# Kernel optimization log

Hardware: AMD Instinct MI355X
Metric: run time of the kernel (lower is better)

## Reference

```python
import jax, jax.numpy as jnp
import numpy as np

N, D, NS, HID = 65536, 256, 1024, 256
EPS = 1e-8
SCALE = D ** -0.5


def layer_norm(x, w, b, eps=1e-5):
    mu = jnp.mean(x, axis=-1, keepdims=True)
    var = jnp.mean(jnp.square(x - mu), axis=-1, keepdims=True)
    return (x - mu) * jax.lax.rsqrt(var + eps) * w + b


def mask_attn(attn, k):
    # per-row top-k mask, vectorized (replaces the torch Python loop)
    idx = jax.lax.top_k(attn, k)[1]                      # [rows, k]
    rows = jnp.arange(attn.shape[0])[:, None]
    mask = jnp.zeros(attn.shape, jnp.bool_).at[rows, idx].set(True)
    return attn * mask


def setup_inputs() -> dict:
    key = jax.random.key(0)
    ks = jax.random.split(key, 20)
    def lin_w(k, din, dout):
        return jax.random.normal(k, (din, dout), jnp.float32) * (1.0 / np.sqrt(din))
    return {
        "inputs": jax.random.normal(ks[0], (N, D), jnp.float32),
        "noise": jax.random.normal(ks[1], (NS, D), jnp.float32),
        "edges_mu": jax.random.normal(ks[2], (1, D), jnp.float32),
        "edges_logsigma": jax.random.uniform(ks[3], (1, D), jnp.float32, -0.1, 0.1),
        "wq": lin_w(ks[4], D, D), "bq": jnp.zeros((D,), jnp.float32),
        "wk": lin_w(ks[5], D, D), "bk": jnp.zeros((D,), jnp.float32),
        "wv": lin_w(ks[6], D, D), "bv": jnp.zeros((D,), jnp.float32),
        "mlp_w1": lin_w(ks[7], 2 * D, HID), "mlp_b1": jnp.zeros((HID,), jnp.float32),
        "mlp_w2": lin_w(ks[8], HID, D), "mlp_b2": jnp.zeros((D,), jnp.float32),
        "ln_in_w": jnp.ones((D,), jnp.float32), "ln_in_b": jnp.zeros((D,), jnp.float32),
        "ln_e_w": jnp.ones((D,), jnp.float32), "ln_e_b": jnp.zeros((D,), jnp.float32),
        "k_n": 512,
        "k_e": 32,
    }


def reference(inputs, noise, edges_mu, edges_logsigma, wq, bq, wk, bk, wv, bv,
              mlp_w1, mlp_b1, mlp_w2, mlp_b2, ln_in_w, ln_in_b, ln_e_w, ln_e_b,
              k_n, k_e):
    # slot init: mu + sigma * eps
    edges = edges_mu + jnp.exp(edges_logsigma) * noise            # [NS, D]
    x = layer_norm(inputs, ln_in_w, ln_in_b)                      # [N, D]
    k = jax.nn.relu(x @ wk + bk)                                  # [N, D]
    v = jax.nn.relu(x @ wv + bv)                                  # [N, D]

    # iters = 1 (single unrolled iteration, as in the default config)
    e = layer_norm(edges, ln_e_w, ln_e_b)                         # [NS, D]
    q = jax.nn.relu(e @ wq + bq)                                  # [NS, D]
    dots = (q @ k.T) * SCALE                                      # [NS, N]
    attn = jax.nn.softmax(dots, axis=1) + EPS
    attn = attn / jnp.sum(attn, axis=1, keepdims=True)
    attn = mask_attn(attn, k_n)
    updates = attn @ v                                            # [NS, D]
    edges = jax.nn.relu(jnp.concatenate([e, updates], axis=1) @ mlp_w1 + mlp_b1) @ mlp_w2 + mlp_b2  # [NS, D]

    q2 = x @ wq + bq                                              # [N, D] (no relu, as in source)
    k2 = jax.nn.relu(edges @ wk + bk)                             # [NS, D]
    dots2 = (q2 @ k2.T) * SCALE                                   # [N, NS]
    H = mask_attn(jax.nn.softmax(dots2, axis=1), k_e)             # [N, NS]
    return edges, H, dots2
```

## Files before the change

kernel.cpp:

```cpp
#include <hip/hip_runtime.h>
#include <hip/hip_bf16.h>
#include <stdint.h>


#define DEV __device__ __forceinline__

typedef uint32_t u32;
typedef uint16_t u16;
typedef __bf16 v8bf __attribute__((ext_vector_type(8)));
typedef float v4f __attribute__((ext_vector_type(4)));

static constexpr long NN = 65536;
static constexpr long DD = 256;
static constexpr long NSL = 1024;

DEV u16 f2b(float f) {
  u32 u = __builtin_bit_cast(u32, f);
  u32 r = (u + 0x7FFFu + ((u >> 16) & 1u)) >> 16;
  return (u16)r;
}
DEV float b2f(u16 h) { u32 u = ((u32)h) << 16; return __builtin_bit_cast(float, u); }
DEV u32 b2k(u32 b) { return b ^ (0x8000u + 0x7FFFu * (b >> 15)); }
DEV float k2fv(u32 k) {
  u16 b = (k & 0x8000u) ? (u16)(k ^ 0x8000u) : (u16)(k ^ 0xFFFFu);
  return b2f(b);
}

DEV void gl_lds16(const u16* g, u16* l) {
  __builtin_amdgcn_global_load_lds(
      (const __attribute__((address_space(1))) u32*)g,
      (__attribute__((address_space(3))) u32*)l, 16, 0, 0);
}

template <int EPI>
__global__ __launch_bounds__(256, 2)
void gemm_bt(const u16* __restrict__ A, const u16* __restrict__ B,
             const float* __restrict__ bias, float scale,
             u16* __restrict__ ob0, u16* __restrict__ ob1, u16* __restrict__ ob2,
             float* __restrict__ of) {
  __shared__ __align__(16) u16 smem[128 * 128];
  u16* As = smem;
  u16* Bs = smem + 128 * 64;
  const int tid = threadIdx.x;
  const int lane = tid & 63;
  const int l15 = lane & 15;
  const int l4 = lane >> 4;
  const int wid = tid >> 6;
  const int wm = wid >> 1, wn = wid & 1;
  const long m0 = (long)blockIdx.y * 128;
  const long n0 = (long)blockIdx.x * 128;

  v4f acc[4][4] = {};

  for (int kb = 0; kb < 256; kb += 64) {
    __syncthreads();
#pragma unroll
    for (int i = 0; i < 4; i++) {
      int cid = tid + 256 * i;
      int row = cid >> 3, ch = cid & 7;
      int sch = ch ^ (row & 7);
      gl_lds16(A + (m0 + row) * 256 + kb + sch * 8, &As[cid * 8]);
      gl_lds16(B + (n0 + row) * 256 + kb + sch * 8, &Bs[cid * 8]);
    }
    __syncthreads();
#pragma unroll
    for (int ks = 0; ks < 2; ks++) {
      v8bf af[4], bfr[4];
#pragma unroll
      for (int m = 0; m < 4; m++) {
        int row = wm * 64 + m * 16 + l15;
        int sch = (ks * 4 + l4) ^ (row & 7);
        af[m] = *reinterpret_cast<const v8bf*>(&As[row * 64 + sch * 8]);
      }
#pragma unroll
      for (int n = 0; n < 4; n++) {
        int row = wn * 64 + n * 16 + l15;
        int sch = (ks * 4 + l4) ^ (row & 7);
        bfr[n] = *reinterpret_cast<const v8bf*>(&Bs[row * 64 + sch * 8]);
      }
#pragma unroll
      for (int m = 0; m < 4; m++)
#pragma unroll
        for (int n = 0; n < 4; n++)
          acc[m][n] = __builtin_amdgcn_mfma_f32_16x16x32_bf16(af[m], bfr[n], acc[m][n], 0, 0, 0);
    }
  }

  const int r4 = l4 * 4;
  if constexpr (EPI == 3) {
#pragma unroll
    for (int m = 0; m < 4; m++)
#pragma unroll
      for (int n = 0; n < 4; n++)
#pragma unroll
        for (int r = 0; r < 4; r++) {
          long grow = m0 + wm * 64 + m * 16 + r4 + r;
          long gcol = n0 + wn * 64 + n * 16 + l15;
          of[grow * 1024 + gcol] = acc[m][n][r] * scale;
        }
  } else {
    __syncthreads();
#pragma unroll
    for (int m = 0; m < 4; m++) {
#pragma unroll
      for (int n = 0; n < 4; n++) {
#pragma unroll
        for (int r = 0; r < 4; r++) {
          int srow = wm * 64 + m * 16 + r4 + r;
          int scol = wn * 64 + n * 16 + l15;
          float v = acc[m][n][r];
          if constexpr (EPI == 0 || EPI == 1) {
            v += bias[n0 + scol];
          } else {
            v *= scale;
          }
          smem[srow * 128 + scol] = f2b(v);
        }
      }
    }
    __syncthreads();
    if constexpr (EPI == 0) {
      const int which = (int)(n0 >> 8);
      const long jj0 = n0 & 255;
      u16* ob = (which == 0) ? ob0 : (which == 1) ? ob1 : ob2;
      const bool dorelu = (which < 2);
#pragma unroll
      for (int i = 0; i < 8; i++) {
        int idx = tid + 256 * i;
        int row = idx >> 4, seg = idx & 15;
        uint4 t = *reinterpret_cast<const uint4*>(&smem[row * 128 + seg * 8]);
        if (dorelu) {
          u32* w = reinterpret_cast<u32*>(&t);
#pragma unroll
          for (int q = 0; q < 4; q++) {
            u32 lo16 = w[q] & 0xffffu, hi16 = w[q] >> 16;
            if (lo16 & 0x8000u) lo16 = 0;
            if (hi16 & 0x8000u) hi16 = 0;
            w[q] = lo16 | (hi16 << 16);
          }
        }
        *reinterpret_cast<uint4*>(&ob[(m0 + row) * 256 + jj0 + seg * 8]) = t;
      }
    } else if constexpr (EPI == 1) {
#pragma unroll
      for (int i = 0; i < 8; i++) {
        int idx = tid + 256 * i;
        int row = idx >> 4, seg = idx & 15;
        uint4 t = *reinterpret_cast<const uint4*>(&smem[row * 128 + seg * 8]);
        u32* w = reinterpret_cast<u32*>(&t);
#pragma unroll
        for (int q = 0; q < 4; q++) {
          u32 lo16 = w[q] & 0xffffu, hi16 = w[q] >> 16;
          if (lo16 & 0x8000u) lo16 = 0;
          if (hi16 & 0x8000u) hi16 = 0;
          w[q] = lo16 | (hi16 << 16);
        }
        *reinterpret_cast<uint4*>(&ob0[(m0 + row) * 256 + n0 + seg * 8]) = t;
      }
    } else {
#pragma unroll
      for (int i = 0; i < 8; i++) {
        int idx = tid + 256 * i;
        int row = idx >> 4, seg = idx & 15;
        uint4 t = *reinterpret_cast<const uint4*>(&smem[row * 128 + seg * 8]);
        *reinterpret_cast<uint4*>(&ob0[(m0 + row) * 65536 + n0 + seg * 8]) = t;
      }
    }
  }
}

__global__ __launch_bounds__(256)
void prep_w_kernel(const float* __restrict__ wq, const float* __restrict__ wk,
                   const float* __restrict__ wv, const float* __restrict__ bq,
                   const float* __restrict__ bk, const float* __restrict__ bv,
                   u16* __restrict__ wcat, float* __restrict__ bcat) {
  int n = blockIdx.x;
  int t = threadIdx.x;
  const float* W = (n < 256) ? wk : (n < 512) ? wv : wq;
  int jj = n & 255;
  wcat[n * 256 + t] = f2b(W[t * 256 + jj]);
  if (t == 0) {
    const float* Bb = (n < 256) ? bk : (n < 512) ? bv : bq;
    bcat[n] = Bb[jj];
  }
}

__global__ __launch_bounds__(256)
void ln_x_kernel(const float* __restrict__ x, const float* __restrict__ lw,
                 const float* __restrict__ lb, u16* __restrict__ out) {
  const int lane = threadIdx.x & 63, wid = threadIdx.x >> 6;
  const long row = (long)blockIdx.x * 4 + wid;
  float4 v = reinterpret_cast<const float4*>(x + row * 256)[lane];
  float s = v.x + v.y + v.z + v.w;
  for (int sh = 1; sh < 64; sh <<= 1) s += __shfl_xor(s, sh);
  float mu = s * (1.f / 256.f);
  float dx = v.x - mu, dy = v.y - mu, dz = v.z - mu, dw = v.w - mu;
  float q = dx * dx + dy * dy + dz * dz + dw * dw;
  for (int sh = 1; sh < 64; sh <<= 1) q += __shfl_xor(q, sh);
  float rs = rsqrtf(q * (1.f / 256.f) + 1e-5f);
  float4 wv = reinterpret_cast<const float4*>(lw)[lane];
  float4 bv = reinterpret_cast<const float4*>(lb)[lane];
  ushort4 o4;
  o4.x = f2b(dx * rs * wv.x + bv.x);
  o4.y = f2b(dy * rs * wv.y + bv.y);
  o4.z = f2b(dz * rs * wv.z + bv.z);
  o4.w = f2b(dw * rs * wv.w + bv.w);
  reinterpret_cast<ushort4*>(out + row * 256)[lane] = o4;
}

__global__ __launch_bounds__(256)
void edges_e_kernel(const float* __restrict__ noise, const float* __restrict__ emu,
                    const float* __restrict__ els, const float* __restrict__ lw,
                    const float* __restrict__ lb, float* __restrict__ e_f,
                    u16* __restrict__ e_b) {
  const int lane = threadIdx.x & 63, wid = threadIdx.x >> 6;
  const long row = (long)blockIdx.x * 4 + wid;
  float4 nz = reinterpret_cast<const float4*>(noise + row * 256)[lane];
  float4 mu4 = reinterpret_cast<const float4*>(emu)[lane];
  float4 ls4 = reinterpret_cast<const float4*>(els)[lane];
  float4 ed;
  ed.x = mu4.x + expf(ls4.x) * nz.x;
  ed.y = mu4.y + expf(ls4.y) * nz.y;
  ed.z = mu4.z + expf(ls4.z) * nz.z;
  ed.w = mu4.w + expf(ls4.w) * nz.w;
  float s = ed.x + ed.y + ed.z + ed.w;
  for (int sh = 1; sh < 64; sh <<= 1) s += __shfl_xor(s, sh);
  float mu = s * (1.f / 256.f);
  float dx = ed.x - mu, dy = ed.y - mu, dz = ed.z - mu, dw = ed.w - mu;
  float qv = dx * dx + dy * dy + dz * dz + dw * dw;
  for (int sh = 1; sh < 64; sh <<= 1) qv += __shfl_xor(qv, sh);
  float rs = rsqrtf(qv * (1.f / 256.f) + 1e-5f);
  float4 wv = reinterpret_cast<const float4*>(lw)[lane];
  float4 bv = reinterpret_cast<const float4*>(lb)[lane];
  float4 ef;
  ef.x = dx * rs * wv.x + bv.x;
  ef.y = dy * rs * wv.y + bv.y;
  ef.z = dz * rs * wv.z + bv.z;
  ef.w = dw * rs * wv.w + bv.w;
  reinterpret_cast<float4*>(e_f + row * 256)[lane] = ef;
  ushort4 o4;
  o4.x = f2b(ef.x); o4.y = f2b(ef.y); o4.z = f2b(ef.z); o4.w = f2b(ef.w);
  reinterpret_cast<ushort4*>(e_b + row * 256)[lane] = o4;
}

struct D2Shm {
  u32 hist[256 * 16];
  u32 c_hi[256];
  u32 sel_idx[1152];
  float sel_w[1152];
  float fred[4];
  u32 sb_star, sThi, sThr;
  float sSE, sFrac;
  u32 scnt;
};

__global__ __launch_bounds__(256, 5)
void d2d3_kernel(const u16* __restrict__ dots, const u16* __restrict__ vmat,
                 const int* __restrict__ knp, float* __restrict__ upd) {
  __shared__ D2Shm S;
  const int tid = threadIdx.x, lane = tid & 63, wid = tid >> 6;
  const int hc = (lane >> 2);
  const long r = blockIdx.x;
  const int kn = *knp;

  for (int i = tid; i < 4096; i += 256) S.hist[i] = 0;
  if (tid == 0) S.scnt = 0;
  __syncthreads();

  const float C = 8.f;
  const uint4* src = reinterpret_cast<const uint4*>(dots + r * 65536);

  float se = 0.f;
  for (int c = tid; c < 8192; c += 256) {
    uint4 d = src[c];
    u32 h[8] = {d.x & 0xffffu, d.x >> 16, d.y & 0xffffu, d.y >> 16,
                d.z & 0xffffu, d.z >> 16, d.w & 0xffffu, d.w >> 16};
#pragma unroll
    for (int j = 0; j < 8; j++) {
      u32 k = b2k(h[j]);
      se += __expf(b2f((u16)h[j]) - C);
      atomicAdd(&S.hist[(k >> 8) * 16 + hc], 1u);
    }
  }
  for (int sh = 1; sh < 64; sh <<= 1) se += __shfl_xor(se, sh);
  if (lane == 0) S.fred[wid] = se;
  __syncthreads();

  {
    u32 s = 0;
#pragma unroll
    for (int c = 0; c < 16; c++) s += S.hist[tid * 16 + c];
    S.c_hi[tid] = s;
  }
  __syncthreads();

  if (tid < 64) {
    u32 s = S.c_hi[4 * tid] + S.c_hi[4 * tid + 1] + S.c_hi[4 * tid + 2] + S.c_hi[4 * tid + 3];
    u32 v = s;
    for (int off = 1; off < 64; off <<= 1) {
      u32 t = (u32)__shfl_down((int)v, off);
      if (tid + off < 64) v += t;
    }
    u32 excl = v - s;
    if (v >= (u32)kn && excl < (u32)kn) {
      u32 acc = excl;
#pragma unroll
      for (int bb = 3; bb >= 0; --bb) {
        int b = 4 * tid + bb;
        u32 nb = acc + S.c_hi[b];
        if (nb >= (u32)kn) { S.sb_star = (u32)b; S.sThi = acc; break; }
        acc = nb;
      }
    }
  } else {
    for (int i = tid - 64; i < 4096; i += 192) S.hist[i] = 0;
  }
  __syncthreads();
  const u32 bstar = S.sb_star;

  for (int c = tid; c < 8192; c += 256) {
    uint4 d = src[c];
    u32 h[8] = {d.x & 0xffffu, d.x >> 16, d.y & 0xffffu, d.y >> 16,
                d.z & 0xffffu, d.z >> 16, d.w & 0xffffu, d.w >> 16};
#pragma unroll
    for (int j = 0; j < 8; j++) {
      u32 k = b2k(h[j]);
      if ((k >> 8) == bstar) atomicAdd(&S.hist[(k & 255u) * 16 + hc], 1u);
    }
  }
  __syncthreads();
  {
    u32 s = 0;
#pragma unroll
    for (int c = 0; c < 16; c++) s += S.hist[tid * 16 + c];
    S.c_hi[tid] = s;
  }
  __syncthreads();

  if (tid < 64) {
    u32 s = S.c_hi[4 * tid] + S.c_hi[4 * tid + 1] + S.c_hi[4 * tid + 2] + S.c_hi[4 * tid + 3];
    u32 v = s;
    for (int off = 1; off < 64; off <<= 1) {
      u32 t = (u32)__shfl_down((int)v, off);
      if (tid + off < 64) v += t;
    }
    const u32 Thi = S.sThi;
    u32 incl = v + Thi;
    u32 excl = v - s + Thi;
    if (incl >= (u32)kn && excl < (u32)kn) {
      u32 acc = excl;
#pragma unroll
      for (int bb = 3; bb >= 0; --bb) {
        int b = 4 * tid + bb;
        u32 nb = acc + S.c_hi[b];
        if (nb >= (u32)kn) {
          S.sThr = (bstar << 8) | (u32)b;
          S.sFrac = (float)(int)((u32)kn - acc) / (float)S.c_hi[b];
          break;
        }
        acc = nb;
      }
    }
    if (tid == 0) {
      float SE = S.fred[0] + S.fred[1] + S.fred[2] + S.fred[3];
      S.sSE = SE;
    }
  }
  __syncthreads();
  const u32 thr = S.sThr;
  const float frac = S.sFrac;
  const float invs = 1.f / S.sSE;
  const float wnorm = 1.f / (1.f + 65536.f * 1e-8f);

  for (int c = tid; c < 8192; c += 256) {
    uint4 d = src[c];
    u32 h[8] = {d.x & 0xffffu, d.x >> 16, d.y & 0xffffu, d.y >> 16,
                d.z & 0xffffu, d.z >> 16, d.w & 0xffffu, d.w >> 16};
#pragma unroll
    for (int j = 0; j < 8; j++) {
      u32 k = b2k(h[j]);
      if (k >= thr) {
        float w = (__expf(k2fv(k) - C) * invs + 1e-8f) * wnorm;
        if (k == thr) w *= frac;
        u32 p = atomicAdd(&S.scnt, 1u);
        if (p < 1152u) { S.sel_idx[p] = (u32)c * 8u + (u32)j; S.sel_w[p] = w; }
      }
    }
  }
  __syncthreads();
  const u32 nsel = S.scnt < 1152u ? S.scnt : 1152u;

  const int g = tid >> 6;
  const int c0 = (tid & 63) * 4;
  float a0 = 0.f, a1 = 0.f, a2 = 0.f, a3 = 0.f;
  float b0 = 0.f, b1 = 0.f, b2 = 0.f, b3 = 0.f;
  u32 j = (u32)g;
  for (; j + 4 < nsel; j += 8) {
    u32 i0 = S.sel_idx[j];      float w0 = S.sel_w[j];
    u32 i1 = S.sel_idx[j + 4];  float w1 = S.sel_w[j + 4];
    ushort4 v0 = *reinterpret_cast<const ushort4*>(vmat + (long)i0 * 256 + c0);
    ushort4 v1 = *reinterpret_cast<const ushort4*>(vmat + (long)i1 * 256 + c0);
    a0 = fmaf(w0, b2f(v0.x), a0); a1 = fmaf(w0, b2f(v0.y), a1);
    a2 = fmaf(w0, b2f(v0.z), a2); a3 = fmaf(w0, b2f(v0.w), a3);
    b0 = fmaf(w1, b2f(v1.x), b0); b1 = fmaf(w1, b2f(v1.y), b1);
    b2 = fmaf(w1, b2f(v1.z), b2); b3 = fmaf(w1, b2f(v1.w), b3);
  }
  for (; j < nsel; j += 4) {
    u32 i0 = S.sel_idx[j];  float w0 = S.sel_w[j];
    ushort4 v0 = *reinterpret_cast<const ushort4*>(vmat + (long)i0 * 256 + c0);
    a0 = fmaf(w0, b2f(v0.x), a0); a1 = fmaf(w0, b2f(v0.y), a1);
    a2 = fmaf(w0, b2f(v0.z), a2); a3 = fmaf(w0, b2f(v0.w), a3);
  }
  __syncthreads();
  float* part = reinterpret_cast<float*>(S.hist);
  float4 pv;
  pv.x = a0 + b0; pv.y = a1 + b1; pv.z = a2 + b2; pv.w = a3 + b3;
  *reinterpret_cast<float4*>(&part[g * 256 + c0]) = pv;
  __syncthreads();
  upd[r * 256 + tid] = part[tid] + part[256 + tid] + part[512 + tid] + part[768 + tid];
}

__global__ __launch_bounds__(256)
void mlp_kernel(const float* __restrict__ e, const float* __restrict__ upd,
                const float* __restrict__ w1, const float* __restrict__ b1,
                const float* __restrict__ w2, const float* __restrict__ b2,
                float* __restrict__ eout, u16* __restrict__ eb) {
  __shared__ float ecat[512];
  __shared__ float h[256];
  const int t = threadIdx.x;
  const long r = blockIdx.x;
  ecat[t] = e[r * 256 + t];
  ecat[256 + t] = upd[r * 256 + t];
  __syncthreads();
  float acc = b1[t];
#pragma unroll 8
  for (int kk = 0; kk < 512; ++kk) acc = fmaf(ecat[kk], w1[kk * 256 + t], acc);
  h[t] = fmaxf(acc, 0.f);
  __syncthreads();
  float a2 = b2[t];
#pragma unroll 8
  for (int kk = 0; kk < 256; ++kk) a2 = fmaf(h[kk], w2[kk * 256 + t], a2);
  eout[r * 256 + t] = a2;
  eb[r * 256 + t] = f2b(a2);
}

__global__ __launch_bounds__(256)
void g2_kernel(const float* __restrict__ d2, const int* __restrict__ kep,
               float* __restrict__ H) {
  const int lane = threadIdx.x & 63, wid = threadIdx.x >> 6;
  const long row = (long)blockIdx.x * 4 + wid;
  const int ke = *kep;
  const float4* src = reinterpret_cast<const float4*>(d2 + row * 1024);
  float4 q0 = src[lane], q1 = src[64 + lane], q2v = src[128 + lane], q3 = src[192 + lane];
  float x[16] = {q0.x, q0.y, q0.z, q0.w, q1.x, q1.y, q1.z, q1.w,
                 q2v.x, q2v.y, q2v.z, q2v.w, q3.x, q3.y, q3.z, q3.w};
  float mx = x[0];
#pragma unroll
  for (int i = 1; i < 16; i++) mx = fmaxf(mx, x[i]);
  for (int sh = 1; sh < 64; sh <<= 1) mx = fmaxf(mx, __shfl_xor(mx, sh));
  float p[16];
  float se = 0.f;
#pragma unroll
  for (int i = 0; i < 16; i++) { p[i] = __expf(x[i] - mx); se += p[i]; }
  for (int sh = 1; sh < 64; sh <<= 1) se += __shfl_xor(se, sh);
  const float invs = 1.f / se;
  u32 key[16];
#pragma unroll
  for (int i = 0; i < 16; i++) key[i] = b2k((u32)f2b(x[i]));
  u32 lo = 0;
  for (int b = 15; b >= 0; --b) {
    u32 t = lo | (1u << b);
    int cnt = 0;
#pragma unroll
    for (int i = 0; i < 16; i++) cnt += (key[i] >= t);
    for (int sh = 1; sh < 64; sh <<= 1) cnt += __shfl_xor(cnt, sh);
    if (cnt >= ke) lo = t;
  }
  float4 o0, o1, o2, o3;
  o0.x = key[0] >= lo ? p[0] * invs : 0.f;
  o0.y = key[1] >= lo ? p[1] * invs : 0.f;
  o0.z = key[2] >= lo ? p[2] * invs : 0.f;
  o0.w = key[3] >= lo ? p[3] * invs : 0.f;
  o1.x = key[4] >= lo ? p[4] * invs : 0.f;
  o1.y = key[5] >= lo ? p[5] * invs : 0.f;
  o1.z = key[6] >= lo ? p[6] * invs : 0.f;
  o1.w = key[7] >= lo ? p[7] * invs : 0.f;
  o2.x = key[8] >= lo ? p[8] * invs : 0.f;
  o2.y = key[9] >= lo ? p[9] * invs : 0.f;
  o2.z = key[10] >= lo ? p[10] * invs : 0.f;
  o2.w = key[11] >= lo ? p[11] * invs : 0.f;
  o3.x = key[12] >= lo ? p[12] * invs : 0.f;
  o3.y = key[13] >= lo ? p[13] * invs : 0.f;
  o3.z = key[14] >= lo ? p[14] * invs : 0.f;
  o3.w = key[15] >= lo ? p[15] * invs : 0.f;
  float4* dst = reinterpret_cast<float4*>(H + row * 1024);
  dst[lane] = o0;
  dst[64 + lane] = o1;
  dst[128 + lane] = o2;
  dst[192 + lane] = o3;
}

extern "C" void kernel_launch(void* const* d_in, const int* in_sizes, int n_in,
                              void* d_out, int out_size, void* d_ws, size_t ws_size,
                              hipStream_t stream) {
  (void)in_sizes; (void)n_in; (void)out_size; (void)ws_size;

  float* out = (float*)d_out;
  float* out_edges = out;
  float* out_H = out + NSL * DD;
  float* out_d2 = out_H + NN * NSL;

  char* Hb = (char*)out_H;
  u16* dots = (u16*)Hb;
  u16* q2b = (u16*)(Hb + 134217728L);
  char* smb = Hb + 167772160L;
  u16* wcat = (u16*)smb;      smb += 768 * 256 * 2;
  float* bcat = (float*)smb;  smb += 4096;
  float* e_f = (float*)smb;   smb += 1024 * 256 * 4;
  u16* e_b = (u16*)smb;       smb += 1024 * 256 * 2;
  u16* q_b = (u16*)smb;       smb += 1024 * 256 * 2;
  float* updf = (float*)smb;  smb += 1024 * 256 * 4;
  u16* edg_b = (u16*)smb;     smb += 1024 * 256 * 2;
  char* Db = (char*)out_d2;
  u16* xln = (u16*)Db;
  u16* kb_ = (u16*)(Db + 33554432L);
  u16* vb_ = (u16*)(Db + 67108864L);
  u16* k2ws = (u16*)d_ws;

  prep_w_kernel<<<768, 256, 0, stream>>>(
      (const float*)d_in[4], (const float*)d_in[6], (const float*)d_in[8],
      (const float*)d_in[5], (const float*)d_in[7], (const float*)d_in[9], wcat, bcat);
  edges_e_kernel<<<256, 256, 0, stream>>>(
      (const float*)d_in[1], (const float*)d_in[2], (const float*)d_in[3],
      (const float*)d_in[16], (const float*)d_in[17], e_f, e_b);
  ln_x_kernel<<<16384, 256, 0, stream>>>(
      (const float*)d_in[0], (const float*)d_in[14], (const float*)d_in[15], xln);
  gemm_bt<1><<<dim3(2, 8), 256, 0, stream>>>(e_b, wcat + 512 * 256, bcat + 512, 1.f,
                                             q_b, nullptr, nullptr, nullptr);
  gemm_bt<0><<<dim3(6, 512), 256, 0, stream>>>(xln, wcat, bcat, 1.f,
                                               kb_, vb_, q2b, nullptr);
  gemm_bt<2><<<dim3(512, 8), 256, 0, stream>>>(q_b, kb_, nullptr, 0.0625f,
                                               dots, nullptr, nullptr, nullptr);
  d2d3_kernel<<<1024, 256, 0, stream>>>(dots, vb_, (const int*)d_in[18], updf);
  mlp_kernel<<<1024, 256, 0, stream>>>(e_f, updf,
                                       (const float*)d_in[10], (const float*)d_in[11],
                                       (const float*)d_in[12], (const float*)d_in[13],
                                       out_edges, edg_b);
  gemm_bt<1><<<dim3(2, 8), 256, 0, stream>>>(edg_b, wcat, bcat, 1.f,
                                             k2ws, nullptr, nullptr, nullptr);
  gemm_bt<3><<<dim3(8, 512), 256, 0, stream>>>(q2b, k2ws, nullptr, 0.0625f,
                                               nullptr, nullptr, nullptr, out_d2);
  g2_kernel<<<16384, 256, 0, stream>>>(out_d2, (const int*)d_in[19], out_H);
}
```

Before: 517.5 us.

## Restructure top-k radix select to 11/5-bit split with candidate buffering

The top-k selection in the softmax/mask kernel now uses a 2048-bin first-pass histogram on the upper 11 bits, and its second pass both emits definite winners and buffers candidates from the boundary bin in shared memory. The third full pass over the 64K-element dots row is then replaced by a scan over the buffered candidates, with a fallback full pass when the buffer overflows. This removes one global read of each row and shrinks the second histogram, at the cost of more shared memory (occupancy hint lowered from 5 to 4) and fewer per-lane histogram copies, so atomics contend more.

```diff
diff --git a/kernel.cpp b/kernel.cpp
--- a/kernel.cpp
+++ b/kernel.cpp
@@ -244,27 +244,26 @@
 }
 
 struct D2Shm {
-  u32 hist[256 * 16];
-  u32 c_hi[256];
+  u32 hist[2048 * 2];
+  u32 chist[2048];
   u32 sel_idx[1152];
   float sel_w[1152];
   float fred[4];
-  u32 sb_star, sThi, sThr;
+  u32 sB, sThi, sThr;
   float sSE, sFrac;
-  u32 scnt;
+  u32 scnt, ccnt;
 };
 
-__global__ __launch_bounds__(256, 5)
+__global__ __launch_bounds__(256, 4)
 void d2d3_kernel(const u16* __restrict__ dots, const u16* __restrict__ vmat,
                  const int* __restrict__ knp, float* __restrict__ upd) {
   __shared__ D2Shm S;
   const int tid = threadIdx.x, lane = tid & 63, wid = tid >> 6;
-  const int hc = (lane >> 2);
+  const int cp = lane >> 5;
   const long r = blockIdx.x;
-  const int kn = *knp;
+  const u32 kn = (u32)(*knp);
 
   for (int i = tid; i < 4096; i += 256) S.hist[i] = 0;
-  if (tid == 0) S.scnt = 0;
   __syncthreads();
 
   const float C = 8.f;
@@ -279,44 +278,49 @@
     for (int j = 0; j < 8; j++) {
       u32 k = b2k(h[j]);
       se += __expf(b2f((u16)h[j]) - C);
-      atomicAdd(&S.hist[(k >> 8) * 16 + hc], 1u);
+      atomicAdd(&S.hist[(k >> 5) * 2 + cp], 1u);
     }
   }
   for (int sh = 1; sh < 64; sh <<= 1) se += __shfl_xor(se, sh);
   if (lane == 0) S.fred[wid] = se;
   __syncthreads();
 
-  {
+  for (int i = tid; i < 2048; i += 256)
+    S.chist[i] = S.hist[i * 2] + S.hist[i * 2 + 1];
+  __syncthreads();
+
+  if (tid < 64) {
     u32 s = 0;
-#pragma unroll
-    for (int c = 0; c < 16; c++) s += S.hist[tid * 16 + c];
-    S.c_hi[tid] = s;
-  }
-  __syncthreads();
-
-  if (tid < 64) {
-    u32 s = S.c_hi[4 * tid] + S.c_hi[4 * tid + 1] + S.c_hi[4 * tid + 2] + S.c_hi[4 * tid + 3];
+    for (int b = tid * 32; b < tid * 32 + 32; b++) s += S.chist[b];
     u32 v = s;
     for (int off = 1; off < 64; off <<= 1) {
       u32 t = (u32)__shfl_down((int)v, off);
       if (tid + off < 64) v += t;
     }
     u32 excl = v - s;
-    if (v >= (u32)kn && excl < (u32)kn) {
+    if (v >= kn && excl < kn) {
       u32 acc = excl;
-#pragma unroll
-      for (int bb = 3; bb >= 0; --bb) {
-        int b = 4 * tid + bb;
-        u32 nb = acc + S.c_hi[b];
-        if (nb >= (u32)kn) { S.sb_star = (u32)b; S.sThi = acc; break; }
+      for (int bb = 31; bb >= 0; --bb) {
+        int b = tid * 32 + bb;
+        u32 nb = acc + S.chist[b];
+        if (nb >= kn) { S.sB = (u32)b; S.sThi = acc; break; }
         acc = nb;
       }
     }
-  } else {
-    for (int i = tid - 64; i < 4096; i += 192) S.hist[i] = 0;
-  }
-  __syncthreads();
-  const u32 bstar = S.sb_star;
+    if (tid == 0) S.sSE = S.fred[0] + S.fred[1] + S.fred[2] + S.fred[3];
+  } else if (tid < 192) {
+    for (int i = tid - 64; i < 512; i += 128) S.hist[2560 + i] = 0;
+  } else if (tid == 255) {
+    S.scnt = 0; S.ccnt = 0;
+  }
+  __syncthreads();
+  const u32 B = S.sB;
+  const u32 Thi = S.sThi;
+  const float invs = 1.f / S.sSE;
+  const float wnorm = 1.f / (1.f + 65536.f * 1e-8f);
+  u32* cand = S.hist;
+  u32* h32 = S.hist + 2560;
+  const int hc16 = lane >> 2;
 
   for (int c = tid; c < 8192; c += 256) {
     uint4 d = src[c];
@@ -325,65 +329,66 @@
 #pragma unroll
     for (int j = 0; j < 8; j++) {
       u32 k = b2k(h[j]);
-      if ((k >> 8) == bstar) atomicAdd(&S.hist[(k & 255u) * 16 + hc], 1u);
-    }
-  }
-  __syncthreads();
-  {
+      u32 p = k >> 5;
+      if (p > B) {
+        float w = (__expf(k2fv(k) - C) * invs + 1e-8f) * wnorm;
+        u32 pos = atomicAdd(&S.scnt, 1u);
+        if (pos < 1152u) { S.sel_idx[pos] = (u32)c * 8u + (u32)j; S.sel_w[pos] = w; }
+      } else if (p == B) {
+        atomicAdd(&h32[(k & 31u) * 16 + hc16], 1u);
+        u32 cc = atomicAdd(&S.ccnt, 1u);
+        if (cc < 2560u) cand[cc] = (((u32)c * 8u + (u32)j) << 16) | (k & 0xffffu);
+      }
+    }
+  }
+  __syncthreads();
+
+  if (tid < 32) {
     u32 s = 0;
 #pragma unroll
-    for (int c = 0; c < 16; c++) s += S.hist[tid * 16 + c];
-    S.c_hi[tid] = s;
-  }
-  __syncthreads();
-
-  if (tid < 64) {
-    u32 s = S.c_hi[4 * tid] + S.c_hi[4 * tid + 1] + S.c_hi[4 * tid + 2] + S.c_hi[4 * tid + 3];
+    for (int c2 = 0; c2 < 16; c2++) s += h32[tid * 16 + c2];
     u32 v = s;
-    for (int off = 1; off < 64; off <<= 1) {
+    for (int off = 1; off < 32; off <<= 1) {
       u32 t = (u32)__shfl_down((int)v, off);
-      if (tid + off < 64) v += t;
-    }
-    const u32 Thi = S.sThi;
+      if (tid + off < 32) v += t;
+    }
     u32 incl = v + Thi;
     u32 excl = v - s + Thi;
-    if (incl >= (u32)kn && excl < (u32)kn) {
-      u32 acc = excl;
-#pragma unroll
-      for (int bb = 3; bb >= 0; --bb) {
-        int b = 4 * tid + bb;
-        u32 nb = acc + S.c_hi[b];
-        if (nb >= (u32)kn) {
-          S.sThr = (bstar << 8) | (u32)b;
-          S.sFrac = (float)(int)((u32)kn - acc) / (float)S.c_hi[b];
-          break;
-        }
-        acc = nb;
-      }
-    }
-    if (tid == 0) {
-      float SE = S.fred[0] + S.fred[1] + S.fred[2] + S.fred[3];
-      S.sSE = SE;
+    if (incl >= kn && excl < kn) {
+      S.sThr = (B << 5) | (u32)tid;
+      S.sFrac = (float)(int)(kn - excl) / (float)s;
     }
   }
   __syncthreads();
   const u32 thr = S.sThr;
   const float frac = S.sFrac;
-  const float invs = 1.f / S.sSE;
-  const float wnorm = 1.f / (1.f + 65536.f * 1e-8f);
-
-  for (int c = tid; c < 8192; c += 256) {
-    uint4 d = src[c];
-    u32 h[8] = {d.x & 0xffffu, d.x >> 16, d.y & 0xffffu, d.y >> 16,
-                d.z & 0xffffu, d.z >> 16, d.w & 0xffffu, d.w >> 16};
-#pragma unroll
-    for (int j = 0; j < 8; j++) {
-      u32 k = b2k(h[j]);
+  const u32 NC = S.ccnt;
+
+  if (NC <= 2560u) {
+    for (u32 i = tid; i < NC; i += 256) {
+      u32 e = cand[i];
+      u32 k = e & 0xffffu;
       if (k >= thr) {
         float w = (__expf(k2fv(k) - C) * invs + 1e-8f) * wnorm;
         if (k == thr) w *= frac;
-        u32 p = atomicAdd(&S.scnt, 1u);
-        if (p < 1152u) { S.sel_idx[p] = (u32)c * 8u + (u32)j; S.sel_w[p] = w; }
+        u32 pos = atomicAdd(&S.scnt, 1u);
+        if (pos < 1152u) { S.sel_idx[pos] = e >> 16; S.sel_w[pos] = w; }
+      }
+    }
+  } else {
+    for (int c = tid; c < 8192; c += 256) {
+      uint4 d = src[c];
+      u32 h[8] = {d.x & 0xffffu, d.x >> 16, d.y & 0xffffu, d.y >> 16,
+                  d.z & 0xffffu, d.z >> 16, d.w & 0xffffu, d.w >> 16};
+#pragma unroll
+      for (int j = 0; j < 8; j++) {
+        u32 k = b2k(h[j]);
+        if ((k >> 5) == B && k >= thr) {
+          float w = (__expf(k2fv(k) - C) * invs + 1e-8f) * wnorm;
+          if (k == thr) w *= frac;
+          u32 pos = atomicAdd(&S.scnt, 1u);
+          if (pos < 1152u) { S.sel_idx[pos] = (u32)c * 8u + (u32)j; S.sel_w[pos] = w; }
+        }
       }
     }
   }
@@ -412,7 +417,7 @@
     a2 = fmaf(w0, b2f(v0.z), a2); a3 = fmaf(w0, b2f(v0.w), a3);
   }
   __syncthreads();
-  float* part = reinterpret_cast<float*>(S.hist);
+  float* part = reinterpret_cast<float*>(S.chist);
   float4 pv;
   pv.x = a0 + b0; pv.y = a1 + b1; pv.z = a2 + b2; pv.w = a3 + b3;
   *reinterpret_cast<float4*>(&part[g * 256 + c0]) = pv;
```

New measurement: 614.9 us. +18.8%, slower.
